# Optimization experiments

Measured on AMD Instinct MI355X. Metric: run time of the kernel, lower is better.

Reference implementation:

```python
import jax, jax.numpy as jnp
import numpy as np
from jax.scipy.special import logsumexp

N, S, D, C = 64, 512, 768, 32


def setup_inputs() -> dict:
    key = jax.random.key(0)
    k1, k2, k3, k4, k5 = jax.random.split(key, 5)
    X = jax.random.normal(k1, (N, S, D), dtype=jnp.float32)
    W = jax.random.normal(k2, (D, C), dtype=jnp.float32) * 0.02
    T = jax.random.normal(k3, (C, C), dtype=jnp.float32) * 0.1
    # one-hot labels [N,S,C]
    lab_idx = jax.random.randint(k4, (N, S), 0, C)
    labels = jax.nn.one_hot(lab_idx, C, dtype=jnp.float32)
    # pad_mask: 1 for first `length` positions, 0 after (lengths in [S//2, S])
    lengths = jax.random.randint(k5, (N,), S // 2, S + 1)
    pad_mask = (jnp.arange(S)[None, :] < lengths[:, None]).astype(jnp.float32)
    return {"X": X, "W": W, "T": T, "labels": labels, "pad_mask": pad_mask}


def _crf_nll(X, W, T, labels, pad_mask):
    npots = jnp.einsum("nsd,dc->nsc", X, W)  # [N,S,C]
    m = pad_mask[..., None]                   # [N,S,1]

    # Faithful replication of the in-place masking loop:
    # prev starts as the ORIGINAL last timestep (t-1 == -1 at t=0 in torch).
    def prop(prev, xs):
        nt, mt = xs
        new = (1.0 - mt) * prev + mt * nt
        return new, new

    _, np_t = jax.lax.scan(
        prop, npots[:, -1, :],
        (jnp.swapaxes(npots, 0, 1), jnp.swapaxes(m, 0, 1)))
    npots = jnp.swapaxes(np_t, 0, 1)  # [N,S,C]

    # Backward messages: msgs[i,j] = lse_k(np[i+1,k] + T[j,k] + msgs[i+1,k]) * mask[i+1]
    def bwd(msg_next, xs):
        np_next, m_next = xs  # [N,C], [N,1]
        new = logsumexp(np_next[:, None, :] + T[None, :, :] + msg_next[:, None, :],
                        axis=-1) * m_next
        return new, new

    xs = (jnp.swapaxes(npots[:, 1:, :], 0, 1), jnp.swapaxes(m[:, 1:, :], 0, 1))
    init = jnp.zeros((npots.shape[0], npots.shape[2]), dtype=npots.dtype)
    _, msgs = jax.lax.scan(bwd, init, xs, reverse=True)
    bwd0 = msgs[0]  # message at position 0

    logZ = logsumexp(npots[:, 0, :] + bwd0, axis=-1)  # [N]

    # Unnormalized gold-path score
    score = jnp.sum(jnp.sum(npots * labels, axis=-1) * pad_mask, axis=-1)
    labels_idx = jnp.argmax(labels, axis=-1)          # [N,S]
    trans = T[labels_idx[:, :-1]]                     # [N,S-1,C]
    score = score + jnp.sum(
        jnp.sum(trans * labels[:, 1:, :], axis=-1) * pad_mask[:, 1:], axis=-1)

    return -jnp.mean(score - logZ)


def reference(X, W, T, labels, pad_mask):
    return _crf_nll(X, W, T, labels, pad_mask)
```

## Files before the change

kernel.cpp:

```cpp
#include <hip/hip_runtime.h>
#include <hip/hip_bf16.h>
#include <math.h>

#define N_ 64
#define S_ 512
#define D_ 768
#define C_ 32
#define KCH 16
#define LC 32
#define WT_LD 776
#define BS_LD 36
#define BS_PER (C_ * BS_LD)

typedef __attribute__((ext_vector_type(8))) short bf16x8;
typedef __attribute__((ext_vector_type(4))) float f32x4;
typedef __attribute__((ext_vector_type(16))) float f32x16;

__device__ inline ushort f2bf(float x) {
    unsigned int b = __builtin_bit_cast(unsigned int, x);
    return (ushort)((b + 0x7FFFu + ((b >> 16) & 1u)) >> 16);
}

__device__ inline unsigned cvt_pk_bf16(float lo, float hi) {
    unsigned r;
    asm("v_cvt_pk_bf16_f32 %0, %1, %2" : "=v"(r) : "v"(lo), "v"(hi));
    return r;
}

__global__ __launch_bounds__(256) void wt_prep(const float* __restrict__ W,
                                               ushort* __restrict__ Wt) {
    const int idx = blockIdx.x * 256 + threadIdx.x;
    if (idx < D_ * C_) {
        const int k = idx >> 5, c = idx & 31;
        Wt[c * WT_LD + k] = f2bf(W[idx]);
    }
}

__global__ __launch_bounds__(256) void gemm_npots_mfma(const float* __restrict__ X,
                                                       const ushort* __restrict__ Wt,
                                                       float* __restrict__ npots) {
    const int tid  = threadIdx.x;
    const int wv   = tid >> 6;
    const int l    = tid & 63;
    const int lr   = l & 15;
    const int q    = l >> 4;
    const int m0   = blockIdx.x * 64 + wv * 16;

    const float*  xrow = X + (size_t)(m0 + lr) * D_ + q * 8;
    const ushort* wb0  = Wt + lr * WT_LD + q * 8;
    const ushort* wb1  = wb0 + 16 * WT_LD;

    f32x4  Aalo[2], Aahi[2], Balo[2], Bahi[2];
    bf16x8 Ab0[2],  Ab1[2],  Bb0[2],  Bb1[2];
    f32x4 acc0 = {0.f, 0.f, 0.f, 0.f};
    f32x4 acc1 = {0.f, 0.f, 0.f, 0.f};

    #define LOADG(S, g)                                                      \
        {                                                                    \
            _Pragma("unroll")                                                \
            for (int j = 0; j < 2; ++j) {                                    \
                const int c_ = (g) * 2 + j;                                  \
                S##alo[j] = *(const f32x4*)(xrow + c_ * 32);                 \
                S##ahi[j] = *(const f32x4*)(xrow + c_ * 32 + 4);             \
                S##b0[j]  = *(const bf16x8*)(wb0 + c_ * 32);                 \
                S##b1[j]  = *(const bf16x8*)(wb1 + c_ * 32);                 \
            }                                                                \
        }

    #define COMPG(S)                                                         \
        {                                                                    \
            _Pragma("unroll")                                                \
            for (int j = 0; j < 2; ++j) {                                    \
                union { unsigned u[4]; bf16x8 v; } af;                       \
                af.u[0] = cvt_pk_bf16(S##alo[j][0], S##alo[j][1]);           \
                af.u[1] = cvt_pk_bf16(S##alo[j][2], S##alo[j][3]);           \
                af.u[2] = cvt_pk_bf16(S##ahi[j][0], S##ahi[j][1]);           \
                af.u[3] = cvt_pk_bf16(S##ahi[j][2], S##ahi[j][3]);           \
                acc0 = __builtin_amdgcn_mfma_f32_16x16x32_bf16(af.v, S##b0[j], acc0, 0, 0, 0); \
                acc1 = __builtin_amdgcn_mfma_f32_16x16x32_bf16(af.v, S##b1[j], acc1, 0, 0, 0); \
            }                                                                \
        }

    LOADG(A, 0);
    LOADG(B, 1);
    for (int g = 0; g < 6; ++g) {
        COMPG(A);
        if (g < 5) LOADG(A, 2 * g + 2);
        COMPG(B);
        if (g < 5) LOADG(B, 2 * g + 3);
    }
    #undef LOADG
    #undef COMPG

    const int r0 = m0 + q * 4;
    #pragma unroll
    for (int reg = 0; reg < 4; ++reg) {
        npots[(size_t)(r0 + reg) * C_ + lr]      = acc0[reg];
        npots[(size_t)(r0 + reg) * C_ + lr + 16] = acc1[reg];
    }
}

__global__ __launch_bounds__(1024) void crf_scan(const float* __restrict__ npots,
                                                 const float* __restrict__ pad,
                                                 const float* __restrict__ T,
                                                 const float* __restrict__ labels,
                                                 float* __restrict__ accum,
                                                 unsigned* __restrict__ cnt_all,
                                                 float* __restrict__ out) {
    __shared__ float e_s[KCH * LC * C_];
    __shared__ float Bs[KCH * BS_PER];
    __shared__ float cls_s[KCH];
    __shared__ float sc_s[KCH];
    __shared__ __align__(16) float wcomb[32];

    const int n   = blockIdx.x;
    const int tid = threadIdx.x;
    const int w   = tid >> 6;
    const int l   = tid & 63;
    const int cc  = l & 31;
    const int h   = l >> 5;

    const float* pm = pad + (size_t)n * S_;
    float lsum = 0.f;
    for (int t = l; t < S_; t += 64) lsum += pm[t];
    #pragma unroll
    for (int o = 32; o >= 1; o >>= 1) lsum += __shfl_xor(lsum, o);
    const int len = (int)(lsum + 0.5f);

    {
        const int k  = w;
        const int lo = k * LC;
        const int hi = min(lo + LC, len - 1);
        float* Bout = &Bs[w * BS_PER];

        if (lo >= len - 1) {
            #pragma unroll
            for (int qq = 0; qq < 16; ++qq) {
                const int row = (qq & 3) + 8 * (qq >> 2) + 4 * h;
                Bout[row * BS_LD + cc] = (row == cc) ? 1.f : 0.f;
            }
            if (l == 0) cls_s[w] = 0.f;
        } else {
            const int cnt = hi - lo;
            float* ew = &e_s[w * (LC * C_)];
            const float* npn = npots + ((size_t)n * S_ + lo) * C_;
            for (int qd = l * 4; qd < cnt * C_; qd += 256) {
                const float4 v = *(const float4*)(npn + qd);
                *(float4*)&ew[qd] = make_float4(expf(v.x), expf(v.y), expf(v.z), expf(v.w));
            }
            asm volatile("s_waitcnt lgkmcnt(0)" ::: "memory");

            float glo[8], ghi[8];
            {
                const float* el = ew + (size_t)(cnt - 1) * C_;
                #pragma unroll
                for (int j = 0; j < 8; ++j) {
                    const int kk = 8 * h + j;
                    glo[j] = el[kk]      * expf(T[kk * C_ + cc]);
                    ghi[j] = el[kk + 16] * expf(T[(kk + 16) * C_ + cc]);
                }
            }

            if (cnt == 1) {
                #pragma unroll
                for (int j = 0; j < 8; ++j) {
                    Bout[(8 * h + j) * BS_LD + cc]        = glo[j];
                    Bout[(8 * h + j + 16) * BS_LD + cc]   = ghi[j];
                }
                if (l == 0) cls_s[w] = 0.f;
            } else {
                union { unsigned u[4]; bf16x8 v; } ETalo, ETahi, blo, bhi;
                #pragma unroll
                for (int t = 0; t < 4; ++t) {
                    const int kk = 8 * h + 2 * t;
                    ETalo.u[t] = cvt_pk_bf16(expf(T[cc * C_ + kk]),      expf(T[cc * C_ + kk + 1]));
                    ETahi.u[t] = cvt_pk_bf16(expf(T[cc * C_ + kk + 16]), expf(T[cc * C_ + kk + 17]));
                    blo.u[t]   = cvt_pk_bf16(glo[2 * t], glo[2 * t + 1]);
                    bhi.u[t]   = cvt_pk_bf16(ghi[2 * t], ghi[2 * t + 1]);
                }

                float logscale = 0.f;
                int it = 0;
                for (int i = hi - 2; i >= lo; --i) {
                    f32x16 d = {};
                    d = __builtin_amdgcn_mfma_f32_32x32x16_bf16(ETalo.v, blo.v, d, 0, 0, 0);
                    d = __builtin_amdgcn_mfma_f32_32x32x16_bf16(ETahi.v, bhi.v, d, 0, 0, 0);

                    const float* ep = ew + (i - lo) * C_ + 4 * h;
                    const float4 e0 = *(const float4*)(ep);
                    const float4 e1 = *(const float4*)(ep + 8);
                    const float4 e2 = *(const float4*)(ep + 16);
                    const float4 e3 = *(const float4*)(ep + 24);
                    float sd[16];
                    sd[0]  = d[0]  * e0.x;  sd[1]  = d[1]  * e0.y;  sd[2]  = d[2]  * e0.z;  sd[3]  = d[3]  * e0.w;
                    sd[4]  = d[4]  * e1.x;  sd[5]  = d[5]  * e1.y;  sd[6]  = d[6]  * e1.z;  sd[7]  = d[7]  * e1.w;
                    sd[8]  = d[8]  * e2.x;  sd[9]  = d[9]  * e2.y;  sd[10] = d[10] * e2.z;  sd[11] = d[11] * e2.w;
                    sd[12] = d[12] * e3.x;  sd[13] = d[13] * e3.y;  sd[14] = d[14] * e3.z;  sd[15] = d[15] * e3.w;

                    if ((++it & 7) == 0) {
                        float m = sd[0];
                        #pragma unroll
                        for (int qq = 1; qq < 16; ++qq) m = fmaxf(m, sd[qq]);
                        #pragma unroll
                        for (int o = 32; o >= 1; o >>= 1) m = fmaxf(m, __shfl_xor(m, o));
                        logscale += logf(m);
                        const float inv = 1.f / m;
                        #pragma unroll
                        for (int qq = 0; qq < 16; ++qq) sd[qq] *= inv;
                    }

                    if (i > lo) {
                        const unsigned w0 = cvt_pk_bf16(sd[0],  sd[1]);
                        const unsigned w1 = cvt_pk_bf16(sd[2],  sd[3]);
                        const unsigned w2 = cvt_pk_bf16(sd[4],  sd[5]);
                        const unsigned w3 = cvt_pk_bf16(sd[6],  sd[7]);
                        const unsigned w4 = cvt_pk_bf16(sd[8],  sd[9]);
                        const unsigned w5 = cvt_pk_bf16(sd[10], sd[11]);
                        const unsigned w6 = cvt_pk_bf16(sd[12], sd[13]);
                        const unsigned w7 = cvt_pk_bf16(sd[14], sd[15]);
                        const unsigned x0 = (unsigned)__shfl_xor((int)w0, 32);
                        const unsigned x1 = (unsigned)__shfl_xor((int)w1, 32);
                        const unsigned x2 = (unsigned)__shfl_xor((int)w2, 32);
                        const unsigned x3 = (unsigned)__shfl_xor((int)w3, 32);
                        const unsigned x4 = (unsigned)__shfl_xor((int)w4, 32);
                        const unsigned x5 = (unsigned)__shfl_xor((int)w5, 32);
                        const unsigned x6 = (unsigned)__shfl_xor((int)w6, 32);
                        const unsigned x7 = (unsigned)__shfl_xor((int)w7, 32);
                        blo.u[0] = h ? x2 : w0;
                        blo.u[1] = h ? x3 : w1;
                        blo.u[2] = h ? w2 : x0;
                        blo.u[3] = h ? w3 : x1;
                        bhi.u[0] = h ? x6 : w4;
                        bhi.u[1] = h ? x7 : w5;
                        bhi.u[2] = h ? w6 : x4;
                        bhi.u[3] = h ? w7 : x5;
                    } else {
                        #pragma unroll
                        for (int qq = 0; qq < 16; ++qq)
                            Bout[((qq & 3) + 8 * (qq >> 2) + 4 * h) * BS_LD + cc] = sd[qq];
                    }
                }
                if (l == 0) cls_s[w] = logscale;
            }
        }
    }

    {
        const int tb = w * LC;
        int best = 0;
        if (l <= LC) {
            const int t = tb - 1 + l;
            if (t >= 0) {
                const float* lrow = labels + ((size_t)n * S_ + t) * C_;
                float bv = lrow[0];
                #pragma unroll
                for (int c = 1; c < C_; ++c) {
                    const float x = lrow[c];
                    if (x > bv) { bv = x; best = c; }
                }
            }
        }
        const int cur = __shfl(best, l + 1);
        float v = 0.f;
        if (l < LC) {
            const int t = tb + l;
            const float p = pad[(size_t)n * S_ + t];
            v = p * npots[((size_t)n * S_ + t) * C_ + cur];
            if (t >= 1) v = fmaf(p, T[best * C_ + cur], v);
        }
        #pragma unroll
        for (int o = 32; o >= 1; o >>= 1) v += __shfl_xor(v, o);
        if (l == 0) sc_s[w] = v;
    }

    __syncthreads();

    if (w == 0) {
        const int r  = l & 31;
        const int hh = l >> 5;

        float cls = (l < KCH) ? cls_s[l] : 0.f;
        #pragma unroll
        for (int o = 32; o >= 1; o >>= 1) cls += __shfl_xor(cls, o);

        float sc = (l < KCH) ? sc_s[l] : 0.f;
        #pragma unroll
        for (int o = 32; o >= 1; o >>= 1) sc += __shfl_xor(sc, o);

        const float np_last = npots[((size_t)n * S_ + (len - 1)) * C_ + r];
        float m0 = np_last;
        #pragma unroll
        for (int o = 32; o >= 1; o >>= 1) m0 = fmaxf(m0, __shfl_xor(m0, o));
        float logscale = m0 + cls;
        if (hh == 0) wcomb[r] = expf(np_last - m0);
        asm volatile("s_waitcnt lgkmcnt(0)" ::: "memory");

        float sn = 0.f;
        for (int k2 = KCH - 1; k2 >= 0; --k2) {
            float cb[16], wv2[16];
            const float* Brow = &Bs[k2 * BS_PER + r * BS_LD + hh * 16];
            #pragma unroll
            for (int t = 0; t < 4; ++t) *(float4*)&cb[t * 4] = *(const float4*)(Brow + t * 4);
            #pragma unroll
            for (int t = 0; t < 4; ++t) *(float4*)&wv2[t * 4] = *(const float4*)&wcomb[hh * 16 + t * 4];
            float s = 0.f;
            #pragma unroll
            for (int t = 0; t < 16; ++t) s = fmaf(cb[t], wv2[t], s);
            s += __shfl_xor(s, 32);

            float m = s;
            #pragma unroll
            for (int o = 16; o >= 1; o >>= 1) m = fmaxf(m, __shfl_xor(m, o));
            logscale += logf(m);
            sn = s / m;
            if (hh == 0) wcomb[r] = sn;
            asm volatile("s_waitcnt lgkmcnt(0)" ::: "memory");
        }
        float vz = (hh == 0) ? sn : 0.f;
        #pragma unroll
        for (int o = 32; o >= 1; o >>= 1) vz += __shfl_xor(vz, o);
        const float logZn = logf(vz) + logscale;

        if (l == 0) {
            atomicAdd(accum, sc - logZn);
            asm volatile("s_waitcnt vmcnt(0)" ::: "memory");
            const unsigned old = atomicAdd(cnt_all, 1u);
            if (old == (unsigned)(N_ - 1)) {
                const float total = atomicAdd(accum, 0.f);
                out[0] = -total / (float)N_;
            }
        }
    }
}

extern "C" void kernel_launch(void* const* d_in, const int* in_sizes, int n_in,
                              void* d_out, int out_size, void* d_ws, size_t ws_size,
                              hipStream_t stream) {
    const float* X      = (const float*)d_in[0];
    const float* W      = (const float*)d_in[1];
    const float* T      = (const float*)d_in[2];
    const float* labels = (const float*)d_in[3];
    const float* pad    = (const float*)d_in[4];
    float* out = (float*)d_out;

    float*    npots   = (float*)d_ws;
    float*    accum   = npots + (size_t)N_ * S_ * C_;
    unsigned* cnt_all = (unsigned*)(accum + 1);
    ushort*   Wt      = (ushort*)(accum + 4);

    hipMemsetAsync(accum, 0, 8, stream);

    wt_prep<<<96, 256, 0, stream>>>(W, Wt);
    gemm_npots_mfma<<<(N_ * S_) / 64, 256, 0, stream>>>(X, Wt, npots);
    crf_scan<<<N_, 1024, 0, stream>>>(npots, pad, T, labels, accum, cnt_all, out);
}
```

Baseline: 61.93 us.

## Fuse W transpose/convert and accumulator reset into GEMM via shared memory

Removes the separate wt_prep kernel and the memset: each GEMM block converts W to bf16 into an LDS-resident transposed copy, and block 0 zeroes the accumulator and counter. Blocks grow to 512 threads covering 128 rows, and B fragments are read from LDS at compute time instead of being prefetched from global memory. This cuts two launches and a dependency on the stream, but every one of the 256 blocks now redoes the 24K-element W conversion, and zeroing accum inside the GEMM relies on it finishing before crf_scan uses it.

```diff
diff --git a/kernel.cpp b/kernel.cpp
--- a/kernel.cpp
+++ b/kernel.cpp
@@ -8,7 +8,7 @@
 #define C_ 32
 #define KCH 16
 #define LC 32
-#define WT_LD 776
+#define WT_LD 772
 #define BS_LD 36
 #define BS_PER (C_ * BS_LD)
 
@@ -27,31 +27,33 @@
     return r;
 }
 
-__global__ __launch_bounds__(256) void wt_prep(const float* __restrict__ W,
-                                               ushort* __restrict__ Wt) {
-    const int idx = blockIdx.x * 256 + threadIdx.x;
-    if (idx < D_ * C_) {
-        const int k = idx >> 5, c = idx & 31;
-        Wt[c * WT_LD + k] = f2bf(W[idx]);
-    }
-}
-
-__global__ __launch_bounds__(256) void gemm_npots_mfma(const float* __restrict__ X,
-                                                       const ushort* __restrict__ Wt,
-                                                       float* __restrict__ npots) {
-    const int tid  = threadIdx.x;
-    const int wv   = tid >> 6;
-    const int l    = tid & 63;
-    const int lr   = l & 15;
-    const int q    = l >> 4;
-    const int m0   = blockIdx.x * 64 + wv * 16;
+__global__ __launch_bounds__(512) void gemm_npots_mfma(const float* __restrict__ X,
+                                                       const float* __restrict__ W,
+                                                       float* __restrict__ npots,
+                                                       float* __restrict__ accum,
+                                                       unsigned* __restrict__ cnt_all) {
+    __shared__ ushort WtS[C_ * WT_LD];
+    const int tid = threadIdx.x;
+
+    if (blockIdx.x == 0 && tid == 0) { accum[0] = 0.f; cnt_all[0] = 0u; }
+
+    for (int i = tid; i < D_ * C_; i += 512) {
+        const int k = i >> 5, c = i & 31;
+        WtS[c * WT_LD + k] = f2bf(W[i]);
+    }
+    __syncthreads();
+
+    const int w  = tid >> 6;
+    const int l  = tid & 63;
+    const int lr = l & 15;
+    const int q  = l >> 4;
+    const int m0 = blockIdx.x * 128 + w * 16;
 
     const float*  xrow = X + (size_t)(m0 + lr) * D_ + q * 8;
-    const ushort* wb0  = Wt + lr * WT_LD + q * 8;
+    const ushort* wb0  = &WtS[lr * WT_LD + q * 8];
     const ushort* wb1  = wb0 + 16 * WT_LD;
 
     f32x4  Aalo[2], Aahi[2], Balo[2], Bahi[2];
-    bf16x8 Ab0[2],  Ab1[2],  Bb0[2],  Bb1[2];
     f32x4 acc0 = {0.f, 0.f, 0.f, 0.f};
     f32x4 acc1 = {0.f, 0.f, 0.f, 0.f};
 
@@ -62,31 +64,32 @@
                 const int c_ = (g) * 2 + j;                                  \
                 S##alo[j] = *(const f32x4*)(xrow + c_ * 32);                 \
                 S##ahi[j] = *(const f32x4*)(xrow + c_ * 32 + 4);             \
-                S##b0[j]  = *(const bf16x8*)(wb0 + c_ * 32);                 \
-                S##b1[j]  = *(const bf16x8*)(wb1 + c_ * 32);                 \
             }                                                                \
         }
 
-    #define COMPG(S)                                                         \
+    #define COMPG(S, g)                                                      \
         {                                                                    \
             _Pragma("unroll")                                                \
             for (int j = 0; j < 2; ++j) {                                    \
+                const int c_ = (g) * 2 + j;                                  \
                 union { unsigned u[4]; bf16x8 v; } af;                       \
                 af.u[0] = cvt_pk_bf16(S##alo[j][0], S##alo[j][1]);           \
                 af.u[1] = cvt_pk_bf16(S##alo[j][2], S##alo[j][3]);           \
                 af.u[2] = cvt_pk_bf16(S##ahi[j][0], S##ahi[j][1]);           \
                 af.u[3] = cvt_pk_bf16(S##ahi[j][2], S##ahi[j][3]);           \
-                acc0 = __builtin_amdgcn_mfma_f32_16x16x32_bf16(af.v, S##b0[j], acc0, 0, 0, 0); \
-                acc1 = __builtin_amdgcn_mfma_f32_16x16x32_bf16(af.v, S##b1[j], acc1, 0, 0, 0); \
+                const bf16x8 b0 = *(const bf16x8*)(wb0 + c_ * 32);           \
+                const bf16x8 b1 = *(const bf16x8*)(wb1 + c_ * 32);           \
+                acc0 = __builtin_amdgcn_mfma_f32_16x16x32_bf16(af.v, b0, acc0, 0, 0, 0); \
+                acc1 = __builtin_amdgcn_mfma_f32_16x16x32_bf16(af.v, b1, acc1, 0, 0, 0); \
             }                                                                \
         }
 
     LOADG(A, 0);
     LOADG(B, 1);
     for (int g = 0; g < 6; ++g) {
-        COMPG(A);
+        COMPG(A, 2 * g);
         if (g < 5) LOADG(A, 2 * g + 2);
-        COMPG(B);
+        COMPG(B, 2 * g + 1);
         if (g < 5) LOADG(B, 2 * g + 3);
     }
     #undef LOADG
@@ -164,8 +167,8 @@
             if (cnt == 1) {
                 #pragma unroll
                 for (int j = 0; j < 8; ++j) {
-                    Bout[(8 * h + j) * BS_LD + cc]        = glo[j];
-                    Bout[(8 * h + j + 16) * BS_LD + cc]   = ghi[j];
+                    Bout[(8 * h + j) * BS_LD + cc]      = glo[j];
+                    Bout[(8 * h + j + 16) * BS_LD + cc] = ghi[j];
                 }
                 if (l == 0) cls_s[w] = 0.f;
             } else {
@@ -346,11 +349,7 @@
     float*    npots   = (float*)d_ws;
     float*    accum   = npots + (size_t)N_ * S_ * C_;
     unsigned* cnt_all = (unsigned*)(accum + 1);
-    ushort*   Wt      = (ushort*)(accum + 4);
-
-    hipMemsetAsync(accum, 0, 8, stream);
-
-    wt_prep<<<96, 256, 0, stream>>>(W, Wt);
-    gemm_npots_mfma<<<(N_ * S_) / 64, 256, 0, stream>>>(X, Wt, npots);
+
+    gemm_npots_mfma<<<(N_ * S_) / 128, 512, 0, stream>>>(X, W, npots, accum, cnt_all);
     crf_scan<<<N_, 1024, 0, stream>>>(npots, pad, T, labels, accum, cnt_all, out);
 }
```

Result: faster. 55.59 us (-10.2%).
